# Kernel tuning notes

Measured on AMD Instinct MI355X. Metric: run time of the kernel, lower is better.

Reference implementation:

```python
import jax, jax.numpy as jnp
import numpy as np

B = 512; NPG = 50; N = B * NPG          # graphs, nodes per graph, total nodes
EPG = 100; E = B * EPG                   # edges per graph, total edges
SPG = 5; S = B * SPG                     # stems per graph, total stems
DIM = 64; FEAT = 24
CONV_STEPS = 12; S2S_STEPS = 3; NSTEM = 105

lrelu = jax.nn.leaky_relu  # negative_slope 0.01, matches nn.LeakyReLU default

def _lin(k, o, i):
    s = 1.0 / np.sqrt(i)
    return jax.random.uniform(k, (o, i), jnp.float32, -s, s)

def _vec(k, o, i):
    s = 1.0 / np.sqrt(i)
    return jax.random.uniform(k, (o,), jnp.float32, -s, s)

def setup_inputs():
    ks = jax.random.split(jax.random.key(0), 30)
    x = jax.random.normal(ks[0], (N, FEAT), jnp.float32)
    edge_attr = jax.random.uniform(ks[1], (E, 4), jnp.float32)
    gid = jnp.arange(E) // EPG
    src = gid * NPG + jax.random.randint(ks[2], (E,), 0, NPG)
    dst = gid * NPG + jax.random.randint(ks[3], (E,), 0, NPG)
    edge_index = jnp.stack([src, dst]).astype(jnp.int32)
    batch = (jnp.arange(N) // NPG).astype(jnp.int32)
    stems = jax.random.randint(ks[4], (S,), 0, NPG).astype(jnp.int32)
    stems_batch = (jnp.arange(S) // SPG).astype(jnp.int32)
    p = dict(
        lin0_w=_lin(ks[5], DIM, FEAT), lin0_b=_vec(ks[6], DIM, FEAT),
        net1_w=_lin(ks[7], 128, 4), net1_b=_vec(ks[8], 128, 4),
        net2_w=_lin(ks[9], DIM * DIM, 128), net2_b=_vec(ks[10], DIM * DIM, 128),
        root_w=_lin(ks[11], DIM, DIM), conv_b=_vec(ks[12], DIM, DIM),
        gru_wih=_lin(ks[13], 3 * DIM, DIM), gru_whh=_lin(ks[14], 3 * DIM, DIM),
        gru_bih=_vec(ks[15], 3 * DIM, DIM), gru_bhh=_vec(ks[16], 3 * DIM, DIM),
        lin1_w=_lin(ks[17], 8 * DIM, DIM), lin1_b=_vec(ks[18], 8 * DIM, DIM),
        lin2_w=_lin(ks[19], NSTEM, 8 * DIM), lin2_b=_vec(ks[20], NSTEM, 8 * DIM),
        lstm_wih=_lin(ks[21], 4 * DIM, 2 * DIM), lstm_whh=_lin(ks[22], 4 * DIM, DIM),
        lstm_bih=_vec(ks[23], 4 * DIM, 2 * DIM), lstm_bhh=_vec(ks[24], 4 * DIM, DIM),
        lin3_w=_lin(ks[25], 1, 2 * DIM), lin3_b=_vec(ks[26], 1, 2 * DIM),
    )
    return dict(x=x, edge_attr=edge_attr, edge_index=edge_index, batch=batch,
                stems=stems, stems_batch=stems_batch, **p)

def reference(x, edge_attr, edge_index, batch, stems, stems_batch,
              lin0_w, lin0_b, net1_w, net1_b, net2_w, net2_b, root_w, conv_b,
              gru_wih, gru_whh, gru_bih, gru_bhh, lin1_w, lin1_b, lin2_w, lin2_b,
              lstm_wih, lstm_whh, lstm_bih, lstm_bhh, lin3_w, lin3_b):
    src, dst = edge_index[0], edge_index[1]
    out = lrelu(x @ lin0_w.T + lin0_b)        # [N, DIM]
    h = out                                   # GRU hidden state
    # edge-conditioned NNConv weights; edge_attr is constant across the 12 steps,
    # so the edge MLP is evaluated once (same math as re-evaluating per step)
    eh = lrelu(edge_attr @ net1_w.T + net1_b)
    W_e = (eh @ net2_w.T + net2_b).reshape(E, DIM, DIM)  # [E, DIM, DIM]
    deg = jax.ops.segment_sum(jnp.ones(E, x.dtype), dst, num_segments=N)
    inv_deg = (1.0 / jnp.maximum(deg, 1.0))[:, None]
    for _ in range(CONV_STEPS):
        msg = jnp.einsum('ed,edo->eo', out[src], W_e)               # gather + per-edge matvec
        agg = jax.ops.segment_sum(msg, dst, num_segments=N) * inv_deg  # scatter-mean
        m = lrelu(agg + out @ root_w + conv_b)                       # NNConv root + bias
        # single GRU step (torch gate order: r, z, n)
        gi = m @ gru_wih.T + gru_bih
        gh = h @ gru_whh.T + gru_bhh
        r = jax.nn.sigmoid(gi[:, :DIM] + gh[:, :DIM])
        z = jax.nn.sigmoid(gi[:, DIM:2 * DIM] + gh[:, DIM:2 * DIM])
        n = jnp.tanh(gi[:, 2 * DIM:] + r * gh[:, 2 * DIM:])
        h = (1.0 - z) * n + z * h
        out = h
    # per-stem head: data.__slices__['x'][stems_batch] + stems with uniform graphs
    stem_idx = stems_batch * NPG + stems
    stem_x = out[stem_idx]
    per_stem = lrelu(stem_x @ lin1_w.T + lin1_b) @ lin2_w.T + lin2_b  # [S, NSTEM]
    # Set2Set pooling: 3 LSTM-attention steps
    q_star = jnp.zeros((B, 2 * DIM), x.dtype)
    hs = jnp.zeros((B, DIM), x.dtype)
    cs = jnp.zeros((B, DIM), x.dtype)
    for _ in range(S2S_STEPS):
        g = q_star @ lstm_wih.T + lstm_bih + hs @ lstm_whh.T + lstm_bhh
        i_g = jax.nn.sigmoid(g[:, :DIM]); f_g = jax.nn.sigmoid(g[:, DIM:2 * DIM])
        c_g = jnp.tanh(g[:, 2 * DIM:3 * DIM]); o_g = jax.nn.sigmoid(g[:, 3 * DIM:])
        cs = f_g * cs + i_g * c_g
        hs = o_g * jnp.tanh(cs)
        e = jnp.sum(out * hs[batch], axis=-1)                        # [N]
        emax = jax.ops.segment_max(e, batch, num_segments=B)
        a = jnp.exp(e - emax[batch])
        a = a / jax.ops.segment_sum(a, batch, num_segments=B)[batch]  # segment softmax
        r_read = jax.ops.segment_sum(a[:, None] * out, batch, num_segments=B)
        q_star = jnp.concatenate([hs, r_read], axis=1)
    sout = q_star @ lin3_w.T + lin3_b   # [B, 1]
    return (per_stem, sout)
```

## Files before the change

### kernel.cpp

```cpp
#include <hip/hip_runtime.h>
#include <hip/hip_bf16.h>
#include <stdint.h>

#define N_NODES 25600
#define N_EDGES 51200
#define NG      512

typedef __attribute__((ext_vector_type(4))) float f32x4;
typedef __attribute__((ext_vector_type(2))) float f32x2;
typedef __attribute__((ext_vector_type(8))) short bf16x8;

typedef union { float4 f4; f32x2 h[2]; } v4u;

__device__ __forceinline__ float lrelu(float v){ return v > 0.f ? v : 0.01f*v; }
__device__ __forceinline__ float sigm(float v){ return 1.f/(1.f+__expf(-v)); }
__device__ __forceinline__ unsigned short f2b(float v){
  union { float f; uint32_t u; } x; x.f = v;
  uint32_t u = x.u;
  return (unsigned short)((u + 0x7FFFu + ((u>>16)&1u)) >> 16);
}
__device__ __forceinline__ unsigned int pk2(float a, float b){
  unsigned int r;
  asm("v_cvt_pk_bf16_f32 %0, %1, %2" : "=v"(r) : "v"(a), "v"(b));
  return r;
}
__device__ __forceinline__ float rl(float v, int l){
  return __int_as_float(__builtin_amdgcn_readlane(__float_as_int(v), l));
}

__global__ void k_prep(const float* __restrict__ net2_w, unsigned short* __restrict__ W2n,
                       const float* __restrict__ gwih, const float* __restrict__ gwhh,
                       float* __restrict__ gw6,
                       const float* __restrict__ lwih, const float* __restrict__ lwhh,
                       float* __restrict__ lwihT, float* __restrict__ lwhhT,
                       const float* __restrict__ lin1w, float* __restrict__ l1T,
                       const float* __restrict__ lin2w, float* __restrict__ l2T,
                       const float* __restrict__ lin0w, float* __restrict__ l0T) {
  const int total = 524288+32768+32768+16384+32768+53760+1536;
  for (int i = blockIdx.x*blockDim.x + threadIdx.x; i < total; i += gridDim.x*blockDim.x) {
    int idx = i;
    if (idx < 524288) {
      int n = idx >> 6, d = idx & 63;
      int k = n >> 6, o = n & 63;
      W2n[idx] = f2b(net2_w[(d*64+o)*128 + k]);
      continue;
    }
    idx -= 524288;
    if (idx < 32768) {
      int dt = idx >> 3, j = idx & 7;
      int d = dt >> 6, t = dt & 63;
      float v = 0.f;
      if (j < 3) v = gwih[(j*64+t)*64 + d];
      else if (j < 6) v = gwhh[((j-3)*64+t)*64 + d];
      gw6[idx] = v; continue;
    }
    idx -= 32768;
    if (idx < 32768) { int c = idx/256, j = idx%256; lwihT[idx] = lwih[j*128+c]; continue; }
    idx -= 32768;
    if (idx < 16384) { int d = idx/256, j = idx%256; lwhhT[idx] = lwhh[j*64+d]; continue; }
    idx -= 16384;
    if (idx < 32768) { int d = idx/512, j = idx%512; l1T[idx] = lin1w[j*64+d]; continue; }
    idx -= 32768;
    if (idx < 53760) { int j = idx/105, o = idx%105; l2T[idx] = lin2w[o*512+j]; continue; }
    idx -= 53760;
    { int f = idx/64, o = idx%64; l0T[idx] = lin0w[o*24+f]; }
  }
}

__global__ __launch_bounds__(256) void k_lin0(const float* __restrict__ x, const float* __restrict__ l0T,
     const float* __restrict__ b, const float* __restrict__ net2_b,
     float* __restrict__ outf, float* __restrict__ Q) {
  int t = threadIdx.x & 63;
  int n = blockIdx.x*4 + (threadIdx.x>>6);
  float xv = (t < 24) ? x[n*24+t] : 0.f;
  float acc = b[t];
  #pragma unroll
  for (int f = 0; f < 24; ++f) acc += __shfl(xv, f) * l0T[f*64+t];
  acc = lrelu(acc);
  outf[n*64+t] = acc;
  float qa = 0.f;
  #pragma unroll 8
  for (int d = 0; d < 64; ++d) qa += __shfl(acc, d) * net2_b[d*64+t];
  Q[n*64+t] = qa;
}

__global__ __launch_bounds__(256) void k_eh(const float* __restrict__ ea, const float* __restrict__ w,
    const float* __restrict__ b, float* __restrict__ ehP) {
  __shared__ float tile[128][65];
  int e0 = blockIdx.x*64;
  int tid = threadIdx.x;
  #pragma unroll
  for (int r = 0; r < 32; ++r) {
    int idx = tid + r*256; int el = idx >> 7, k = idx & 127;
    float4 a = *(const float4*)(ea + (size_t)(e0+el)*4);
    float4 ww = *(const float4*)(w + k*4);
    tile[k][el] = lrelu(a.x*ww.x + a.y*ww.y + a.z*ww.z + a.w*ww.w + b[k]);
  }
  __syncthreads();
  #pragma unroll
  for (int r = 0; r < 32; ++r) {
    int idx = tid + r*256; int k = idx >> 6, el = idx & 63;
    ehP[((size_t)(k>>1)*N_EDGES + e0 + el)*2 + (k&1)] = tile[k][el];
  }
}

__global__ __launch_bounds__(128) void k_csr(const int* __restrict__ ei, int* __restrict__ deg,
                                             int* __restrict__ off, int* __restrict__ csr) {
  __shared__ int cnt[50];
  __shared__ int cur[50];
  __shared__ int dloc[100];
  int g = blockIdx.x, t = threadIdx.x;
  const int* dst = ei + N_EDGES;
  if (t < 50) cnt[t] = 0;
  __syncthreads();
  if (t < 100) { dloc[t] = dst[g*100+t] - g*50; atomicAdd(&cnt[dloc[t]], 1); }
  __syncthreads();
  if (t == 0) { int run = 0; for (int i = 0; i < 50; ++i) { cur[i] = run; run += cnt[i]; } }
  __syncthreads();
  if (t < 50) { deg[g*50+t] = cnt[t]; off[g*50+t] = g*100 + cur[t]; }
  __syncthreads();
  if (t < 100) {
    int p = 0, me = dloc[t];
    for (int i = 0; i < t; ++i) p += (dloc[i] == me);
    csr[g*100 + cur[me] + p] = g*100 + t;
  }
}

__global__ __launch_bounds__(512, 4) void k_step(
    float* __restrict__ outf, const float* __restrict__ ehP,
    const unsigned short* __restrict__ W2n, float* __restrict__ Qb,
    const int* __restrict__ ei, const int* __restrict__ csr,
    const int* __restrict__ offs, const int* __restrict__ deg,
    const float* __restrict__ rootw, const float* __restrict__ conv_b,
    const float* __restrict__ gw6, const float* __restrict__ bih, const float* __restrict__ bhh,
    const float* __restrict__ net2_b) {
  __shared__ __align__(16) char  BtB[128*128];
  __shared__ __align__(16) float Tt[64*132];
  __shared__ f32x2 ehl2[2][112];
  __shared__ int sel[100];
  __shared__ int offl[64];
  __shared__ int degl[64];
  __shared__ float invd[64];
  float* aggL = Tt;

  const int tid = threadIdx.x;
  const int g = blockIdx.x;
  const int wave = tid >> 6, lane = tid & 63;
  const int t = lane;
  const int q = lane >> 4, cc = lane & 15;
  const int mw = wave >> 1, nh = wave & 1;

  if (tid < 64) {
    int dgv = 0, ofv = 0;
    if (tid < 50) { dgv = deg[g*50+tid]; ofv = offs[g*50+tid] - g*100; }
    degl[tid] = dgv; offl[tid] = ofv;
    invd[tid] = 1.f/(float)(dgv > 0 ? dgv : 1);
  }
  if (tid < 100) {
    int eg = csr[g*100+tid];
    sel[tid] = (ei[eg]-g*50) | ((eg-g*100) << 16);
  }
  const int brow = tid >> 2, bpart = tid & 3;
  const float* ehPg = ehP + (size_t)g*100*2;
  int4 br0, br1;
  {
    const unsigned short* src = W2n + (size_t)brow*64 + bpart*16;
    br0 = *(const int4*)src; br1 = *(const int4*)(src + 8);
  }
  f32x2 er = {0.f, 0.f};
  if (tid < 100) er = *(const f32x2*)(ehPg + tid*2);
  __syncthreads();

  const int r = tid >> 3, dq = tid & 7;
  const int myo = offl[r], mydg = degl[r];
  int se0=0, se1=0, se2=0, se3=0;
  if (mydg > 0) se0 = sel[myo];
  if (mydg > 1) se1 = sel[myo+1];
  if (mydg > 2) se2 = sel[myo+2];
  if (mydg > 3) se3 = sel[myo+3];

  bf16x8 xf00, xf01, xf10, xf11;
  {
    int xr0 = nh*32 + cc, xr1 = xr0 + 16;
    union { bf16x8 v; uint u[4]; } X;
    #pragma unroll
    for (int half = 0; half < 4; ++half) {
      int row = (half & 1) ? xr1 : xr0;
      int d0  = (half & 2) ? (32 + q*8) : (q*8);
      if (row < 50) {
        const float* p = outf + (size_t)(g*50+row)*64 + d0;
        float4 a = *(const float4*)p;
        float4 b = *(const float4*)(p+4);
        X.u[0]=pk2(a.x,a.y); X.u[1]=pk2(a.z,a.w); X.u[2]=pk2(b.x,b.y); X.u[3]=pk2(b.z,b.w);
      } else { X.u[0]=0; X.u[1]=0; X.u[2]=0; X.u[3]=0; }
      if (half==0) xf00=X.v; else if (half==1) xf10=X.v; else if (half==2) xf01=X.v; else xf11=X.v;
    }
  }

  *(int4*)(BtB + (brow<<7) + (((bpart*2  )^(brow&7))<<4)) = br0;
  *(int4*)(BtB + (brow<<7) + (((bpart*2+1)^(brow&7))<<4)) = br1;
  if (tid < 100) ehl2[0][tid] = er;
  __syncthreads();

  f32x2 fin01={0,0}, fin23={0,0}, fin45={0,0}, fin67={0,0};

  #pragma unroll 1
  for (int c = 0; c < 64; ++c) {
    f32x4 tc00={}, tc01={}, tc10={}, tc11={};
    {
      int ar0 = mw*32 + cc, ar1 = ar0 + 16;
      #pragma unroll
      for (int ks = 0; ks < 2; ++ks) {
        bf16x8 af0 = *(const bf16x8*)(BtB + (ar0<<7) + (((ks*4+q)^(ar0&7))<<4));
        bf16x8 af1 = *(const bf16x8*)(BtB + (ar1<<7) + (((ks*4+q)^(ar1&7))<<4));
        bf16x8 xb0 = ks ? xf01 : xf00;
        bf16x8 xb1 = ks ? xf11 : xf10;
        tc00 = __builtin_amdgcn_mfma_f32_16x16x32_bf16(af0, xb0, tc00, 0,0,0);
        tc01 = __builtin_amdgcn_mfma_f32_16x16x32_bf16(af0, xb1, tc01, 0,0,0);
        tc10 = __builtin_amdgcn_mfma_f32_16x16x32_bf16(af1, xb0, tc10, 0,0,0);
        tc11 = __builtin_amdgcn_mfma_f32_16x16x32_bf16(af1, xb1, tc11, 0,0,0);
      }
    }
    {
      int n0a = mw*32 + q*4, n0b = n0a + 16;
      int sA = nh*32 + cc,   sB = sA + 16;
      float4 v;
      v.x=tc00[0]; v.y=tc00[1]; v.z=tc00[2]; v.w=tc00[3];
      *(float4*)&Tt[sA*132 + n0a] = v;
      v.x=tc01[0]; v.y=tc01[1]; v.z=tc01[2]; v.w=tc01[3];
      *(float4*)&Tt[sB*132 + n0a] = v;
      v.x=tc10[0]; v.y=tc10[1]; v.z=tc10[2]; v.w=tc10[3];
      *(float4*)&Tt[sA*132 + n0b] = v;
      v.x=tc11[0]; v.y=tc11[1]; v.z=tc11[2]; v.w=tc11[3];
      *(float4*)&Tt[sB*132 + n0b] = v;
    }
    if (c < 63) {
      const unsigned short* src = W2n + ((size_t)(c+1)*128 + brow)*64 + bpart*16;
      br0 = *(const int4*)src; br1 = *(const int4*)(src + 8);
      if (tid < 100) er = *(const f32x2*)(ehPg + (size_t)(c+1)*N_EDGES*2 + tid*2);
    }
    __syncthreads();
    {
      const f32x2* ebuf = ehl2[c & 1];
      for (int ii = 0; ii < mydg; ++ii) {
        int pk = (ii==0)?se0:(ii==1)?se1:(ii==2)?se2:(ii==3)?se3:sel[myo+ii];
        int s2 = pk & 0xffff, e2 = pk >> 16;
        f32x2 ep = ebuf[e2];
        const float* tb = &Tt[s2*132 + dq*8];
        v4u a0, a1, b0, b1;
        a0.f4 = *(const float4*)(tb);
        a1.f4 = *(const float4*)(tb + 4);
        b0.f4 = *(const float4*)(tb + 64);
        b1.f4 = *(const float4*)(tb + 68);
        f32x2 ex = {ep.x, ep.x}, ey = {ep.y, ep.y};
        fin01 += a0.h[0]*ex + b0.h[0]*ey;
        fin23 += a0.h[1]*ex + b0.h[1]*ey;
        fin45 += a1.h[0]*ex + b1.h[0]*ey;
        fin67 += a1.h[1]*ex + b1.h[1]*ey;
      }
    }
    if (c < 63) {
      *(int4*)(BtB + (brow<<7) + (((bpart*2  )^(brow&7))<<4)) = br0;
      *(int4*)(BtB + (brow<<7) + (((bpart*2+1)^(brow&7))<<4)) = br1;
      if (tid < 100) ehl2[(c+1)&1][tid] = er;
    }
    __syncthreads();
  }

  {
    for (int ii = 0; ii < mydg; ++ii) {
      int pk = (ii==0)?se0:(ii==1)?se1:(ii==2)?se2:(ii==3)?se3:sel[myo+ii];
      int s2 = pk & 0xffff;
      const float* qp = Qb + (size_t)(g*50 + s2)*64 + dq*8;
      v4u q0, q1;
      q0.f4 = *(const float4*)(qp);
      q1.f4 = *(const float4*)(qp + 4);
      fin01 += q0.h[0]; fin23 += q0.h[1];
      fin45 += q1.h[0]; fin67 += q1.h[1];
    }
    float4 f0 = {fin01.x, fin01.y, fin23.x, fin23.y};
    float4 f1 = {fin45.x, fin45.y, fin67.x, fin67.y};
    *(float4*)&aggL[r*66 + dq*8]     = f0;
    *(float4*)&aggL[r*66 + dq*8 + 4] = f1;
  }
  __syncthreads();

  {
    float ot[8];
    #pragma unroll
    for (int i = 0; i < 8; ++i) {
      int n = wave*8 + i;
      ot[i] = (n < 50) ? outf[(size_t)(g*50+n)*64 + t] : 0.f;
    }
    float mm[8];
    {
      float rc[8] = {0,0,0,0,0,0,0,0};
      for (int d = 0; d < 64; ++d) {
        float w = rootw[d*64+t];
        #pragma unroll
        for (int i = 0; i < 8; ++i) rc[i] += rl(ot[i], d) * w;
      }
      float cb = conv_b[t];
      #pragma unroll
      for (int i = 0; i < 8; ++i) {
        int n = wave*8 + i;
        mm[i] = lrelu(aggL[n*66 + t]*invd[n] + rc[i] + cb);
      }
    }
    float air[8]={}, aiz[8]={}, ain[8]={}, ahr[8]={}, ahz[8]={}, ahn[8]={};
    for (int d = 0; d < 64; ++d) {
      const float* wp = gw6 + (size_t)(d*64+t)*8;
      float4 w0 = *(const float4*)wp;
      float4 w1 = *(const float4*)(wp + 4);
      #pragma unroll
      for (int i = 0; i < 8; ++i) {
        float md = rl(mm[i], d), hd = rl(ot[i], d);
        air[i] += md*w0.x; aiz[i] += md*w0.y; ain[i] += md*w0.z;
        ahr[i] += hd*w0.w; ahz[i] += hd*w1.x; ahn[i] += hd*w1.y;
      }
    }
    float bi0 = bih[t], bi1 = bih[64+t], bi2 = bih[128+t];
    float bh0 = bhh[t], bh1 = bhh[64+t], bh2 = bhh[128+t];
    float h[8];
    #pragma unroll
    for (int i = 0; i < 8; ++i) {
      int n = wave*8 + i;
      float rg = sigm(air[i] + bi0 + ahr[i] + bh0);
      float zg = sigm(aiz[i] + bi1 + ahz[i] + bh1);
      float ng = tanhf(ain[i] + bi2 + rg*(ahn[i] + bh2));
      h[i] = (1.f - zg)*ng + zg*ot[i];
      if (n < 50) outf[(size_t)(g*50+n)*64 + t] = h[i];
    }
    float qa[8] = {0,0,0,0,0,0,0,0};
    for (int d = 0; d < 64; ++d) {
      float qw = net2_b[d*64+t];
      #pragma unroll
      for (int i = 0; i < 8; ++i) qa[i] += rl(h[i], d) * qw;
    }
    #pragma unroll
    for (int i = 0; i < 8; ++i) {
      int n = wave*8 + i;
      if (n < 50) Qb[(size_t)(g*50+n)*64 + t] = qa[i];
    }
  }
}

__global__ __launch_bounds__(256) void k_stem(const float* __restrict__ outf,
    const int* __restrict__ stems, const int* __restrict__ stems_batch,
    const float* __restrict__ l1T, const float* __restrict__ l1b,
    const float* __restrict__ l2T, const float* __restrict__ l2b,
    float* __restrict__ per_stem) {
  int t = threadIdx.x & 63;
  int s = blockIdx.x*4 + (threadIdx.x>>6);
  int node = stems_batch[s]*50 + stems[s];
  float sx = outf[node*64+t];
  float t1[8];
  #pragma unroll
  for (int g = 0; g < 8; ++g) t1[g] = l1b[g*64+t];
  for (int d = 0; d < 64; ++d) {
    float xd = __shfl(sx, d);
    const float* L = l1T + d*512 + t;
    #pragma unroll
    for (int g = 0; g < 8; ++g) t1[g] += xd * L[g*64];
  }
  #pragma unroll
  for (int g = 0; g < 8; ++g) t1[g] = lrelu(t1[g]);
  float a0 = l2b[t];
  float a1 = (t < 41) ? l2b[64+t] : 0.f;
  for (int g = 0; g < 8; ++g) {
    for (int d = 0; d < 64; ++d) {
      float tj = __shfl(t1[g], d);
      int j = g*64 + d;
      a0 += tj * l2T[j*105 + t];
      a1 += tj * ((t < 41) ? l2T[j*105 + 64 + t] : 0.f);
    }
  }
  per_stem[s*105 + t] = a0;
  if (t < 41) per_stem[s*105 + 64 + t] = a1;
}

__global__ __launch_bounds__(64) void k_s2s(const float* __restrict__ outf,
    const float* __restrict__ wihT, const float* __restrict__ whhT,
    const float* __restrict__ bih, const float* __restrict__ bhh,
    const float* __restrict__ l3w, const float* __restrict__ l3b,
    float* __restrict__ sout) {
  int b = blockIdx.x, t = threadIdx.x;
  const float* og = outf + b*50*64;
  float qlo = 0.f, qhi = 0.f, hs = 0.f, cs = 0.f;
  float b0 = bih[t]+bhh[t], b1 = bih[64+t]+bhh[64+t], b2 = bih[128+t]+bhh[128+t], b3 = bih[192+t]+bhh[192+t];
  for (int it = 0; it < 3; ++it) {
    float g0 = b0, g1 = b1, g2 = b2, g3 = b3;
    for (int c = 0; c < 64; ++c) {
      float qc = __shfl(qlo, c);
      const float* L = wihT + c*256 + t;
      g0 += qc*L[0]; g1 += qc*L[64]; g2 += qc*L[128]; g3 += qc*L[192];
    }
    for (int c = 0; c < 64; ++c) {
      float qc = __shfl(qhi, c);
      const float* L = wihT + (64+c)*256 + t;
      g0 += qc*L[0]; g1 += qc*L[64]; g2 += qc*L[128]; g3 += qc*L[192];
    }
    for (int d = 0; d < 64; ++d) {
      float hd = __shfl(hs, d);
      const float* L = whhT + d*256 + t;
      g0 += hd*L[0]; g1 += hd*L[64]; g2 += hd*L[128]; g3 += hd*L[192];
    }
    float ig = sigm(g0), fg = sigm(g1), cg = tanhf(g2), oo = sigm(g3);
    cs = fg*cs + ig*cg;
    hs = oo*tanhf(cs);
    float ei = -3.4e38f;
    for (int i = 0; i < 50; ++i) {
      float p = og[i*64+t]*hs;
      #pragma unroll
      for (int m2 = 1; m2 < 64; m2 <<= 1) p += __shfl_xor(p, m2);
      if (t == i) ei = p;
    }
    float em = ei;
    #pragma unroll
    for (int m2 = 1; m2 < 64; m2 <<= 1) em = fmaxf(em, __shfl_xor(em, m2));
    float av = (t < 50) ? __expf(ei - em) : 0.f;
    float as = av;
    #pragma unroll
    for (int m2 = 1; m2 < 64; m2 <<= 1) as += __shfl_xor(as, m2);
    av /= as;
    float rr = 0.f;
    for (int i = 0; i < 50; ++i) rr += __shfl(av, i) * og[i*64+t];
    qlo = hs; qhi = rr;
  }
  float p = qlo*l3w[t] + qhi*l3w[64+t];
  #pragma unroll
  for (int m2 = 1; m2 < 64; m2 <<= 1) p += __shfl_xor(p, m2);
  if (t == 0) sout[b] = p + l3b[0];
}

extern "C" void kernel_launch(void* const* d_in, const int* in_sizes, int n_in,
                              void* d_out, int out_size, void* d_ws, size_t ws_size,
                              hipStream_t stream) {
  const float* x          = (const float*)d_in[0];
  const float* edge_attr  = (const float*)d_in[1];
  const int*   edge_index = (const int*)  d_in[2];
  const int*   stems      = (const int*)  d_in[4];
  const int*   stems_b    = (const int*)  d_in[5];
  const float* lin0_w = (const float*)d_in[6];
  const float* lin0_b = (const float*)d_in[7];
  const float* net1_w = (const float*)d_in[8];
  const float* net1_b = (const float*)d_in[9];
  const float* net2_w = (const float*)d_in[10];
  const float* net2_b = (const float*)d_in[11];
  const float* root_w = (const float*)d_in[12];
  const float* conv_b = (const float*)d_in[13];
  const float* gru_wih = (const float*)d_in[14];
  const float* gru_whh = (const float*)d_in[15];
  const float* gru_bih = (const float*)d_in[16];
  const float* gru_bhh = (const float*)d_in[17];
  const float* lin1_w = (const float*)d_in[18];
  const float* lin1_b = (const float*)d_in[19];
  const float* lin2_w = (const float*)d_in[20];
  const float* lin2_b = (const float*)d_in[21];
  const float* lstm_wih = (const float*)d_in[22];
  const float* lstm_whh = (const float*)d_in[23];
  const float* lstm_bih = (const float*)d_in[24];
  const float* lstm_bhh = (const float*)d_in[25];
  const float* lin3_w = (const float*)d_in[26];
  const float* lin3_b = (const float*)d_in[27];

  char* ws = (char*)d_ws;
  size_t off = 0;
  auto alloc = [&](size_t bytes) { void* p = ws + off; off += (bytes + 255) & ~(size_t)255; return p; };
  float* ehP  = (float*)alloc((size_t)N_EDGES*128*4);
  unsigned short* W2n = (unsigned short*)alloc(524288*2);
  float* outf = (float*)alloc((size_t)N_NODES*64*4);
  float* Qb   = (float*)alloc((size_t)N_NODES*64*4);
  int* deg  = (int*)alloc(N_NODES*4);
  int* offs = (int*)alloc(N_NODES*4);
  int* csr  = (int*)alloc(N_EDGES*4);
  float* gw6   = (float*)alloc(32768*4);
  float* lwihT = (float*)alloc(32768*4);
  float* lwhhT = (float*)alloc(16384*4);
  float* l1T   = (float*)alloc(32768*4);
  float* l2T   = (float*)alloc(53760*4);
  float* l0T   = (float*)alloc(1536*4);

  if (off > ws_size) {
    hipMemsetAsync(d_out, 0, (size_t)out_size * sizeof(float), stream);
    return;
  }

  float* per_stem = (float*)d_out;
  float* sout = per_stem + 2560*105;

  k_prep<<<2712, 256, 0, stream>>>(net2_w, W2n, gru_wih, gru_whh, gw6,
                                   lstm_wih, lstm_whh, lwihT, lwhhT,
                                   lin1_w, l1T, lin2_w, l2T, lin0_w, l0T);
  k_lin0<<<N_NODES/4, 256, 0, stream>>>(x, l0T, lin0_b, net2_b, outf, Qb);
  k_eh<<<N_EDGES/64, 256, 0, stream>>>(edge_attr, net1_w, net1_b, ehP);
  k_csr<<<NG, 128, 0, stream>>>(edge_index, deg, offs, csr);
  for (int s = 0; s < 12; ++s) {
    k_step<<<NG, 512, 0, stream>>>(outf, ehP, W2n, Qb, edge_index, csr, offs, deg,
                                   root_w, conv_b, gw6, gru_bih, gru_bhh, net2_b);
  }
  k_stem<<<2560/4, 256, 0, stream>>>(outf, stems, stems_b, l1T, lin1_b, l2T, lin2_b, per_stem);
  k_s2s<<<NG, 64, 0, stream>>>(outf, lwihT, lwhhT, lstm_bih, lstm_bhh, lin3_w, lin3_b, sout);
}
```

Measured before the change: 2.516 ms.

## Fuse all twelve message-passing steps into one persistent per-graph kernel

Replaces the twelve separate step launches with a single kernel that loops over the steps inside each block. The node states and the net2-bias projection Q are kept in shared memory between steps and written to global memory only at the end. This removes launch overhead and the global round-trips of node features and Q; the Q computation also moves out of lin0 into the kernel. The cost is about 25KB more LDS per block, which lowers the number of resident blocks per CU.

```diff
diff --git a/kernel.cpp b/kernel.cpp
--- a/kernel.cpp
+++ b/kernel.cpp
@@ -9,8 +9,6 @@
 typedef __attribute__((ext_vector_type(4))) float f32x4;
 typedef __attribute__((ext_vector_type(2))) float f32x2;
 typedef __attribute__((ext_vector_type(8))) short bf16x8;
-
-typedef union { float4 f4; f32x2 h[2]; } v4u;
 
 __device__ __forceinline__ float lrelu(float v){ return v > 0.f ? v : 0.01f*v; }
 __device__ __forceinline__ float sigm(float v){ return 1.f/(1.f+__expf(-v)); }
@@ -68,20 +66,14 @@
 }
 
 __global__ __launch_bounds__(256) void k_lin0(const float* __restrict__ x, const float* __restrict__ l0T,
-     const float* __restrict__ b, const float* __restrict__ net2_b,
-     float* __restrict__ outf, float* __restrict__ Q) {
+     const float* __restrict__ b, float* __restrict__ outf) {
   int t = threadIdx.x & 63;
   int n = blockIdx.x*4 + (threadIdx.x>>6);
   float xv = (t < 24) ? x[n*24+t] : 0.f;
   float acc = b[t];
   #pragma unroll
   for (int f = 0; f < 24; ++f) acc += __shfl(xv, f) * l0T[f*64+t];
-  acc = lrelu(acc);
-  outf[n*64+t] = acc;
-  float qa = 0.f;
-  #pragma unroll 8
-  for (int d = 0; d < 64; ++d) qa += __shfl(acc, d) * net2_b[d*64+t];
-  Q[n*64+t] = qa;
+  outf[n*64+t] = lrelu(acc);
 }
 
 __global__ __launch_bounds__(256) void k_eh(const float* __restrict__ ea, const float* __restrict__ w,
@@ -126,14 +118,14 @@
   }
 }
 
-__global__ __launch_bounds__(512, 4) void k_step(
+__global__ __launch_bounds__(512, 4) void k_conv(
     float* __restrict__ outf, const float* __restrict__ ehP,
-    const unsigned short* __restrict__ W2n, float* __restrict__ Qb,
+    const unsigned short* __restrict__ W2n,
     const int* __restrict__ ei, const int* __restrict__ csr,
     const int* __restrict__ offs, const int* __restrict__ deg,
     const float* __restrict__ rootw, const float* __restrict__ conv_b,
-    const float* __restrict__ gw6, const float* __restrict__ bih, const float* __restrict__ bhh,
-    const float* __restrict__ net2_b) {
+    const float* __restrict__ gw6, const float* __restrict__ bih,
+    const float* __restrict__ bhh, const float* __restrict__ net2_b) {
   __shared__ __align__(16) char  BtB[128*128];
   __shared__ __align__(16) float Tt[64*132];
   __shared__ f32x2 ehl2[2][112];
@@ -141,6 +133,8 @@
   __shared__ int offl[64];
   __shared__ int degl[64];
   __shared__ float invd[64];
+  __shared__ __align__(16) float hf[50*64];
+  __shared__ __align__(16) float Ql[50*64];
   float* aggL = Tt;
 
   const int tid = threadIdx.x;
@@ -160,15 +154,7 @@
     int eg = csr[g*100+tid];
     sel[tid] = (ei[eg]-g*50) | ((eg-g*100) << 16);
   }
-  const int brow = tid >> 2, bpart = tid & 3;
-  const float* ehPg = ehP + (size_t)g*100*2;
-  int4 br0, br1;
-  {
-    const unsigned short* src = W2n + (size_t)brow*64 + bpart*16;
-    br0 = *(const int4*)src; br1 = *(const int4*)(src + 8);
-  }
-  f32x2 er = {0.f, 0.f};
-  if (tid < 100) er = *(const f32x2*)(ehPg + tid*2);
+  for (int i = tid; i < 3200; i += 512) hf[i] = outf[(size_t)g*3200 + i];
   __syncthreads();
 
   const int r = tid >> 3, dq = tid & 7;
@@ -179,170 +165,208 @@
   if (mydg > 2) se2 = sel[myo+2];
   if (mydg > 3) se3 = sel[myo+3];
 
-  bf16x8 xf00, xf01, xf10, xf11;
   {
-    int xr0 = nh*32 + cc, xr1 = xr0 + 16;
-    union { bf16x8 v; uint u[4]; } X;
-    #pragma unroll
-    for (int half = 0; half < 4; ++half) {
-      int row = (half & 1) ? xr1 : xr0;
-      int d0  = (half & 2) ? (32 + q*8) : (q*8);
-      if (row < 50) {
-        const float* p = outf + (size_t)(g*50+row)*64 + d0;
-        float4 a = *(const float4*)p;
-        float4 b = *(const float4*)(p+4);
-        X.u[0]=pk2(a.x,a.y); X.u[1]=pk2(a.z,a.w); X.u[2]=pk2(b.x,b.y); X.u[3]=pk2(b.z,b.w);
-      } else { X.u[0]=0; X.u[1]=0; X.u[2]=0; X.u[3]=0; }
-      if (half==0) xf00=X.v; else if (half==1) xf10=X.v; else if (half==2) xf01=X.v; else xf11=X.v;
-    }
-  }
-
-  *(int4*)(BtB + (brow<<7) + (((bpart*2  )^(brow&7))<<4)) = br0;
-  *(int4*)(BtB + (brow<<7) + (((bpart*2+1)^(brow&7))<<4)) = br1;
-  if (tid < 100) ehl2[0][tid] = er;
-  __syncthreads();
-
-  f32x2 fin01={0,0}, fin23={0,0}, fin45={0,0}, fin67={0,0};
-
-  #pragma unroll 1
-  for (int c = 0; c < 64; ++c) {
-    f32x4 tc00={}, tc01={}, tc10={}, tc11={};
-    {
-      int ar0 = mw*32 + cc, ar1 = ar0 + 16;
-      #pragma unroll
-      for (int ks = 0; ks < 2; ++ks) {
-        bf16x8 af0 = *(const bf16x8*)(BtB + (ar0<<7) + (((ks*4+q)^(ar0&7))<<4));
-        bf16x8 af1 = *(const bf16x8*)(BtB + (ar1<<7) + (((ks*4+q)^(ar1&7))<<4));
-        bf16x8 xb0 = ks ? xf01 : xf00;
-        bf16x8 xb1 = ks ? xf11 : xf10;
-        tc00 = __builtin_amdgcn_mfma_f32_16x16x32_bf16(af0, xb0, tc00, 0,0,0);
-        tc01 = __builtin_amdgcn_mfma_f32_16x16x32_bf16(af0, xb1, tc01, 0,0,0);
-        tc10 = __builtin_amdgcn_mfma_f32_16x16x32_bf16(af1, xb0, tc10, 0,0,0);
-        tc11 = __builtin_amdgcn_mfma_f32_16x16x32_bf16(af1, xb1, tc11, 0,0,0);
-      }
-    }
-    {
-      int n0a = mw*32 + q*4, n0b = n0a + 16;
-      int sA = nh*32 + cc,   sB = sA + 16;
-      float4 v;
-      v.x=tc00[0]; v.y=tc00[1]; v.z=tc00[2]; v.w=tc00[3];
-      *(float4*)&Tt[sA*132 + n0a] = v;
-      v.x=tc01[0]; v.y=tc01[1]; v.z=tc01[2]; v.w=tc01[3];
-      *(float4*)&Tt[sB*132 + n0a] = v;
-      v.x=tc10[0]; v.y=tc10[1]; v.z=tc10[2]; v.w=tc10[3];
-      *(float4*)&Tt[sA*132 + n0b] = v;
-      v.x=tc11[0]; v.y=tc11[1]; v.z=tc11[2]; v.w=tc11[3];
-      *(float4*)&Tt[sB*132 + n0b] = v;
-    }
-    if (c < 63) {
-      const unsigned short* src = W2n + ((size_t)(c+1)*128 + brow)*64 + bpart*16;
-      br0 = *(const int4*)src; br1 = *(const int4*)(src + 8);
-      if (tid < 100) er = *(const f32x2*)(ehPg + (size_t)(c+1)*N_EDGES*2 + tid*2);
-    }
-    __syncthreads();
-    {
-      const f32x2* ebuf = ehl2[c & 1];
-      for (int ii = 0; ii < mydg; ++ii) {
-        int pk = (ii==0)?se0:(ii==1)?se1:(ii==2)?se2:(ii==3)?se3:sel[myo+ii];
-        int s2 = pk & 0xffff, e2 = pk >> 16;
-        f32x2 ep = ebuf[e2];
-        const float* tb = &Tt[s2*132 + dq*8];
-        v4u a0, a1, b0, b1;
-        a0.f4 = *(const float4*)(tb);
-        a1.f4 = *(const float4*)(tb + 4);
-        b0.f4 = *(const float4*)(tb + 64);
-        b1.f4 = *(const float4*)(tb + 68);
-        f32x2 ex = {ep.x, ep.x}, ey = {ep.y, ep.y};
-        fin01 += a0.h[0]*ex + b0.h[0]*ey;
-        fin23 += a0.h[1]*ex + b0.h[1]*ey;
-        fin45 += a1.h[0]*ex + b1.h[0]*ey;
-        fin67 += a1.h[1]*ex + b1.h[1]*ey;
-      }
-    }
-    if (c < 63) {
-      *(int4*)(BtB + (brow<<7) + (((bpart*2  )^(brow&7))<<4)) = br0;
-      *(int4*)(BtB + (brow<<7) + (((bpart*2+1)^(brow&7))<<4)) = br1;
-      if (tid < 100) ehl2[(c+1)&1][tid] = er;
-    }
-    __syncthreads();
-  }
-
-  {
-    for (int ii = 0; ii < mydg; ++ii) {
-      int pk = (ii==0)?se0:(ii==1)?se1:(ii==2)?se2:(ii==3)?se3:sel[myo+ii];
-      int s2 = pk & 0xffff;
-      const float* qp = Qb + (size_t)(g*50 + s2)*64 + dq*8;
-      v4u q0, q1;
-      q0.f4 = *(const float4*)(qp);
-      q1.f4 = *(const float4*)(qp + 4);
-      fin01 += q0.h[0]; fin23 += q0.h[1];
-      fin45 += q1.h[0]; fin67 += q1.h[1];
-    }
-    float4 f0 = {fin01.x, fin01.y, fin23.x, fin23.y};
-    float4 f1 = {fin45.x, fin45.y, fin67.x, fin67.y};
-    *(float4*)&aggL[r*66 + dq*8]     = f0;
-    *(float4*)&aggL[r*66 + dq*8 + 4] = f1;
-  }
-  __syncthreads();
-
-  {
-    float ot[8];
+    float hcur[8];
     #pragma unroll
     for (int i = 0; i < 8; ++i) {
       int n = wave*8 + i;
-      ot[i] = (n < 50) ? outf[(size_t)(g*50+n)*64 + t] : 0.f;
-    }
-    float mm[8];
-    {
-      float rc[8] = {0,0,0,0,0,0,0,0};
-      for (int d = 0; d < 64; ++d) {
-        float w = rootw[d*64+t];
-        #pragma unroll
-        for (int i = 0; i < 8; ++i) rc[i] += rl(ot[i], d) * w;
-      }
-      float cb = conv_b[t];
-      #pragma unroll
-      for (int i = 0; i < 8; ++i) {
-        int n = wave*8 + i;
-        mm[i] = lrelu(aggL[n*66 + t]*invd[n] + rc[i] + cb);
-      }
-    }
-    float air[8]={}, aiz[8]={}, ain[8]={}, ahr[8]={}, ahz[8]={}, ahn[8]={};
-    for (int d = 0; d < 64; ++d) {
-      const float* wp = gw6 + (size_t)(d*64+t)*8;
-      float4 w0 = *(const float4*)wp;
-      float4 w1 = *(const float4*)(wp + 4);
-      #pragma unroll
-      for (int i = 0; i < 8; ++i) {
-        float md = rl(mm[i], d), hd = rl(ot[i], d);
-        air[i] += md*w0.x; aiz[i] += md*w0.y; ain[i] += md*w0.z;
-        ahr[i] += hd*w0.w; ahz[i] += hd*w1.x; ahn[i] += hd*w1.y;
-      }
-    }
-    float bi0 = bih[t], bi1 = bih[64+t], bi2 = bih[128+t];
-    float bh0 = bhh[t], bh1 = bhh[64+t], bh2 = bhh[128+t];
-    float h[8];
-    #pragma unroll
-    for (int i = 0; i < 8; ++i) {
-      int n = wave*8 + i;
-      float rg = sigm(air[i] + bi0 + ahr[i] + bh0);
-      float zg = sigm(aiz[i] + bi1 + ahz[i] + bh1);
-      float ng = tanhf(ain[i] + bi2 + rg*(ahn[i] + bh2));
-      h[i] = (1.f - zg)*ng + zg*ot[i];
-      if (n < 50) outf[(size_t)(g*50+n)*64 + t] = h[i];
+      hcur[i] = (n < 50) ? hf[n*64+t] : 0.f;
     }
     float qa[8] = {0,0,0,0,0,0,0,0};
     for (int d = 0; d < 64; ++d) {
       float qw = net2_b[d*64+t];
       #pragma unroll
-      for (int i = 0; i < 8; ++i) qa[i] += rl(h[i], d) * qw;
+      for (int i = 0; i < 8; ++i) qa[i] += rl(hcur[i], d) * qw;
     }
     #pragma unroll
     for (int i = 0; i < 8; ++i) {
       int n = wave*8 + i;
-      if (n < 50) Qb[(size_t)(g*50+n)*64 + t] = qa[i];
-    }
-  }
+      if (n < 50) Ql[n*64+t] = qa[i];
+    }
+  }
+  __syncthreads();
+
+  const float* ehPg = ehP + (size_t)g*100*2;
+  const int brow = tid >> 2, bpart = tid & 3;
+  const int n0a = mw*32 + q*4, n0b = n0a + 16;
+  const int sA = nh*32 + cc,   sB = sA + 16;
+
+  #pragma unroll 1
+  for (int s = 0; s < 12; ++s) {
+    int4 br0, br1;
+    {
+      const unsigned short* src = W2n + (size_t)brow*64 + bpart*16;
+      br0 = *(const int4*)src; br1 = *(const int4*)(src + 8);
+    }
+    f32x2 er = {0.f, 0.f};
+    if (tid < 100) er = *(const f32x2*)(ehPg + tid*2);
+
+    bf16x8 xf00, xf01, xf10, xf11;
+    {
+      int xr0 = nh*32 + cc, xr1 = xr0 + 16;
+      union { bf16x8 v; uint u[4]; } X;
+      #pragma unroll
+      for (int half = 0; half < 4; ++half) {
+        int row = (half & 1) ? xr1 : xr0;
+        int d0  = (half & 2) ? (32 + q*8) : (q*8);
+        if (row < 50) {
+          const float* p = &hf[row*64 + d0];
+          float4 a = *(const float4*)p;
+          float4 b = *(const float4*)(p+4);
+          X.u[0]=pk2(a.x,a.y); X.u[1]=pk2(a.z,a.w); X.u[2]=pk2(b.x,b.y); X.u[3]=pk2(b.z,b.w);
+        } else { X.u[0]=0; X.u[1]=0; X.u[2]=0; X.u[3]=0; }
+        if (half==0) xf00=X.v; else if (half==1) xf10=X.v; else if (half==2) xf01=X.v; else xf11=X.v;
+      }
+    }
+
+    *(int4*)(BtB + (brow<<7) + (((bpart*2  )^(brow&7))<<4)) = br0;
+    *(int4*)(BtB + (brow<<7) + (((bpart*2+1)^(brow&7))<<4)) = br1;
+    if (tid < 100) ehl2[0][tid] = er;
+    __syncthreads();
+
+    f32x2 fin01={0,0}, fin23={0,0}, fin45={0,0}, fin67={0,0};
+
+    #pragma unroll 1
+    for (int c = 0; c < 64; ++c) {
+      f32x4 tc00={}, tc01={}, tc10={}, tc11={};
+      {
+        int ar0 = mw*32 + cc, ar1 = ar0 + 16;
+        #pragma unroll
+        for (int ks = 0; ks < 2; ++ks) {
+          bf16x8 af0 = *(const bf16x8*)(BtB + (ar0<<7) + (((ks*4+q)^(ar0&7))<<4));
+          bf16x8 af1 = *(const bf16x8*)(BtB + (ar1<<7) + (((ks*4+q)^(ar1&7))<<4));
+          bf16x8 xb0 = ks ? xf01 : xf00;
+          bf16x8 xb1 = ks ? xf11 : xf10;
+          tc00 = __builtin_amdgcn_mfma_f32_16x16x32_bf16(af0, xb0, tc00, 0,0,0);
+          tc01 = __builtin_amdgcn_mfma_f32_16x16x32_bf16(af0, xb1, tc01, 0,0,0);
+          tc10 = __builtin_amdgcn_mfma_f32_16x16x32_bf16(af1, xb0, tc10, 0,0,0);
+          tc11 = __builtin_amdgcn_mfma_f32_16x16x32_bf16(af1, xb1, tc11, 0,0,0);
+        }
+      }
+      {
+        float4 v;
+        v.x=tc00[0]; v.y=tc00[1]; v.z=tc00[2]; v.w=tc00[3];
+        *(float4*)&Tt[sA*132 + n0a] = v;
+        v.x=tc01[0]; v.y=tc01[1]; v.z=tc01[2]; v.w=tc01[3];
+        *(float4*)&Tt[sB*132 + n0a] = v;
+        v.x=tc10[0]; v.y=tc10[1]; v.z=tc10[2]; v.w=tc10[3];
+        *(float4*)&Tt[sA*132 + n0b] = v;
+        v.x=tc11[0]; v.y=tc11[1]; v.z=tc11[2]; v.w=tc11[3];
+        *(float4*)&Tt[sB*132 + n0b] = v;
+      }
+      if (c < 63) {
+        const unsigned short* src = W2n + ((size_t)(c+1)*128 + brow)*64 + bpart*16;
+        br0 = *(const int4*)src; br1 = *(const int4*)(src + 8);
+        if (tid < 100) er = *(const f32x2*)(ehPg + (size_t)(c+1)*N_EDGES*2 + tid*2);
+      }
+      __syncthreads();
+      {
+        const f32x2* ebuf = ehl2[c & 1];
+        for (int ii = 0; ii < mydg; ++ii) {
+          int pk = (ii==0)?se0:(ii==1)?se1:(ii==2)?se2:(ii==3)?se3:sel[myo+ii];
+          int s2 = pk & 0xffff, e2 = pk >> 16;
+          f32x2 ep = ebuf[e2];
+          const float* tb = &Tt[s2*132 + dq*8];
+          union { float4 f4; f32x2 h[2]; } a0, a1, b0, b1;
+          a0.f4 = *(const float4*)(tb);
+          a1.f4 = *(const float4*)(tb + 4);
+          b0.f4 = *(const float4*)(tb + 64);
+          b1.f4 = *(const float4*)(tb + 68);
+          f32x2 ex = {ep.x, ep.x}, ey = {ep.y, ep.y};
+          fin01 += a0.h[0]*ex + b0.h[0]*ey;
+          fin23 += a0.h[1]*ex + b0.h[1]*ey;
+          fin45 += a1.h[0]*ex + b1.h[0]*ey;
+          fin67 += a1.h[1]*ex + b1.h[1]*ey;
+        }
+      }
+      if (c < 63) {
+        *(int4*)(BtB + (brow<<7) + (((bpart*2  )^(brow&7))<<4)) = br0;
+        *(int4*)(BtB + (brow<<7) + (((bpart*2+1)^(brow&7))<<4)) = br1;
+        if (tid < 100) ehl2[(c+1)&1][tid] = er;
+      }
+      __syncthreads();
+    }
+
+    {
+      for (int ii = 0; ii < mydg; ++ii) {
+        int pk = (ii==0)?se0:(ii==1)?se1:(ii==2)?se2:(ii==3)?se3:sel[myo+ii];
+        int s2 = pk & 0xffff;
+        const float* qp = &Ql[s2*64 + dq*8];
+        union { float4 f4; f32x2 h[2]; } q0, q1;
+        q0.f4 = *(const float4*)(qp);
+        q1.f4 = *(const float4*)(qp + 4);
+        fin01 += q0.h[0]; fin23 += q0.h[1];
+        fin45 += q1.h[0]; fin67 += q1.h[1];
+      }
+      float4 f0 = {fin01.x, fin01.y, fin23.x, fin23.y};
+      float4 f1 = {fin45.x, fin45.y, fin67.x, fin67.y};
+      *(float4*)&aggL[r*66 + dq*8]     = f0;
+      *(float4*)&aggL[r*66 + dq*8 + 4] = f1;
+    }
+    __syncthreads();
+
+    {
+      float ot[8];
+      #pragma unroll
+      for (int i = 0; i < 8; ++i) {
+        int n = wave*8 + i;
+        ot[i] = (n < 50) ? hf[n*64+t] : 0.f;
+      }
+      float mm[8];
+      {
+        float rc[8] = {0,0,0,0,0,0,0,0};
+        for (int d = 0; d < 64; ++d) {
+          float w = rootw[d*64+t];
+          #pragma unroll
+          for (int i = 0; i < 8; ++i) rc[i] += rl(ot[i], d) * w;
+        }
+        float cb = conv_b[t];
+        #pragma unroll
+        for (int i = 0; i < 8; ++i) {
+          int n = wave*8 + i;
+          mm[i] = lrelu(aggL[n*66 + t]*invd[n] + rc[i] + cb);
+        }
+      }
+      float air[8]={}, aiz[8]={}, ain[8]={}, ahr[8]={}, ahz[8]={}, ahn[8]={};
+      for (int d = 0; d < 64; ++d) {
+        const float* wp = gw6 + (size_t)(d*64+t)*8;
+        float4 w0 = *(const float4*)wp;
+        float4 w1 = *(const float4*)(wp + 4);
+        #pragma unroll
+        for (int i = 0; i < 8; ++i) {
+          float md = rl(mm[i], d), hd = rl(ot[i], d);
+          air[i] += md*w0.x; aiz[i] += md*w0.y; ain[i] += md*w0.z;
+          ahr[i] += hd*w0.w; ahz[i] += hd*w1.x; ahn[i] += hd*w1.y;
+        }
+      }
+      float bi0 = bih[t], bi1 = bih[64+t], bi2 = bih[128+t];
+      float bh0 = bhh[t], bh1 = bhh[64+t], bh2 = bhh[128+t];
+      float h[8];
+      #pragma unroll
+      for (int i = 0; i < 8; ++i) {
+        int n = wave*8 + i;
+        float rg = sigm(air[i] + bi0 + ahr[i] + bh0);
+        float zg = sigm(aiz[i] + bi1 + ahz[i] + bh1);
+        float ng = tanhf(ain[i] + bi2 + rg*(ahn[i] + bh2));
+        h[i] = (1.f - zg)*ng + zg*ot[i];
+        if (n < 50) hf[n*64+t] = h[i];
+      }
+      float qa[8] = {0,0,0,0,0,0,0,0};
+      for (int d = 0; d < 64; ++d) {
+        float qw = net2_b[d*64+t];
+        #pragma unroll
+        for (int i = 0; i < 8; ++i) qa[i] += rl(h[i], d) * qw;
+      }
+      #pragma unroll
+      for (int i = 0; i < 8; ++i) {
+        int n = wave*8 + i;
+        if (n < 50) Ql[n*64+t] = qa[i];
+      }
+    }
+    __syncthreads();
+  }
+
+  for (int i = tid; i < 3200; i += 512) outf[(size_t)g*3200 + i] = hf[i];
 }
 
 __global__ __launch_bounds__(256) void k_stem(const float* __restrict__ outf,
@@ -470,7 +494,6 @@
   float* ehP  = (float*)alloc((size_t)N_EDGES*128*4);
   unsigned short* W2n = (unsigned short*)alloc(524288*2);
   float* outf = (float*)alloc((size_t)N_NODES*64*4);
-  float* Qb   = (float*)alloc((size_t)N_NODES*64*4);
   int* deg  = (int*)alloc(N_NODES*4);
   int* offs = (int*)alloc(N_NODES*4);
   int* csr  = (int*)alloc(N_EDGES*4);
@@ -492,13 +515,11 @@
   k_prep<<<2712, 256, 0, stream>>>(net2_w, W2n, gru_wih, gru_whh, gw6,
                                    lstm_wih, lstm_whh, lwihT, lwhhT,
                                    lin1_w, l1T, lin2_w, l2T, lin0_w, l0T);
-  k_lin0<<<N_NODES/4, 256, 0, stream>>>(x, l0T, lin0_b, net2_b, outf, Qb);
+  k_lin0<<<N_NODES/4, 256, 0, stream>>>(x, l0T, lin0_b, outf);
   k_eh<<<N_EDGES/64, 256, 0, stream>>>(edge_attr, net1_w, net1_b, ehP);
   k_csr<<<NG, 128, 0, stream>>>(edge_index, deg, offs, csr);
-  for (int s = 0; s < 12; ++s) {
-    k_step<<<NG, 512, 0, stream>>>(outf, ehP, W2n, Qb, edge_index, csr, offs, deg,
-                                   root_w, conv_b, gw6, gru_bih, gru_bhh, net2_b);
-  }
+  k_conv<<<NG, 512, 0, stream>>>(outf, ehP, W2n, edge_index, csr, offs, deg,
+                                 root_w, conv_b, gw6, gru_bih, gru_bhh, net2_b);
   k_stem<<<2560/4, 256, 0, stream>>>(outf, stems, stems_b, l1T, lin1_b, l2T, lin2_b, per_stem);
   k_s2s<<<NG, 64, 0, stream>>>(outf, lwihT, lwhhT, lstm_bih, lstm_bhh, lin3_w, lin3_b, sout);
 }
```

Result: faster. 2.407 ms (-4.3%).
